# Performance work log

Measured on AMD Instinct MI355X. Metric: run time of the kernel, lower is better.

The kernel has to match this reference:

```python
import jax, jax.numpy as jnp
import numpy as np


def setup_inputs() -> dict:
    key = jax.random.key(0)
    ks = jax.random.split(key, 8)
    B, S, Nc, C, Cseed = 4, 4096, 8192, 512, 256
    return {
        "query_xyz": jax.random.normal(ks[0], (B, S, 3), dtype=jnp.float32),
        "ref_xyz": jax.random.normal(ks[1], (B, Nc, 3), dtype=jnp.float32),
        "ref_feat": jax.random.normal(ks[2], (B, C, Nc), dtype=jnp.float32),
        "seed_features": jax.random.normal(ks[3], (B, Cseed, S), dtype=jnp.float32),
        "W_seed_proj": jax.random.normal(ks[4], (Cseed, C), dtype=jnp.float32) * 0.02,
        "b_seed_proj": jax.random.normal(ks[5], (Cseed,), dtype=jnp.float32) * 0.02,
        "W_concat_proj": jax.random.normal(ks[6], (Cseed, 2 * Cseed), dtype=jnp.float32) * 0.02,
        "b_concat_proj": jax.random.normal(ks[7], (Cseed,), dtype=jnp.float32) * 0.02,
    }


def _nn_gather(query_xyz, ref_xyz, ref_feat):
    # torch.cdist(p=2) + argmin: argmin over squared distance is identical
    # (sqrt is monotonic), so we skip the sqrt.
    q2 = jnp.sum(query_xyz * query_xyz, axis=-1, keepdims=True)      # (B,S,1)
    r2 = jnp.sum(ref_xyz * ref_xyz, axis=-1)[:, None, :]             # (B,1,Nc)
    qr = jnp.einsum("bsd,bnd->bsn", query_xyz, ref_xyz)              # (B,S,Nc)
    d2 = q2 + r2 - 2.0 * qr                                          # (B,S,Nc)
    idx = jnp.argmin(d2, axis=-1)                                    # (B,S) int
    # gather nearest-neighbor features: (B,C,Nc) -> (B,C,S)
    return jnp.take_along_axis(ref_feat, idx[:, None, :], axis=2)


def reference(query_xyz, ref_xyz, ref_feat, seed_features,
              W_seed_proj, b_seed_proj, W_concat_proj, b_concat_proj):
    lift3d_raw = _nn_gather(query_xyz, ref_xyz, ref_feat)            # (B,C,S)
    # 1x1 Conv1d == channel matmul
    lift3d_seed = jnp.einsum("oc,bcs->bos", W_seed_proj, lift3d_raw) \
                  + b_seed_proj[None, :, None]                       # (B,256,S)
    fused = jnp.concatenate([seed_features, lift3d_seed], axis=1)    # (B,512,S)
    out = jnp.einsum("oc,bcs->bos", W_concat_proj, fused) \
          + b_concat_proj[None, :, None]                             # (B,256,S)
    return out
```

## Files before the change

### kernel.cpp

```cpp
#include <hip/hip_runtime.h>

#define B_   4
#define S_   4096
#define NC   8192
#define C_   512
#define CS   256
#define KTOT 768

typedef __attribute__((ext_vector_type(8))) short short8;
typedef __attribute__((ext_vector_type(4))) float f32x4;

static __device__ __forceinline__ unsigned short f2bf(float x) {
    unsigned u = __builtin_bit_cast(unsigned, x);
    unsigned r = u + 0x7FFFu + ((u >> 16) & 1u);
    return (unsigned short)(r >> 16);
}

__global__ __launch_bounds__(256) void pad_ref_kernel(const float* __restrict__ rxyz,
                                                      float4* __restrict__ refpk) {
    int gid = blockIdx.x * 256 + threadIdx.x;
    float x = rxyz[gid * 3 + 0];
    float y = rxyz[gid * 3 + 1];
    float z = rxyz[gid * 3 + 2];
    float r2 = __fadd_rn(__fadd_rn(__fmul_rn(x, x), __fmul_rn(y, y)), __fmul_rn(z, z));
    refpk[gid] = make_float4(x, y, z, r2);
}

__global__ __launch_bounds__(256) void argmin_partial_kernel(
        const float* __restrict__ qxyz, const float4* __restrict__ refpk,
        float* __restrict__ pval, int* __restrict__ pidx) {
    int tid = threadIdx.x;
    int lane = tid & 63;
    int qg = tid >> 6;
    int sblk = blockIdx.x;
    int c = blockIdx.y;
    int b = blockIdx.z;
    int sbase = sblk * 32 + qg * 8;

    float qx[8], qy[8], qz[8], q2[8];
    #pragma unroll
    for (int q = 0; q < 8; ++q) {
        const float* qp = qxyz + ((size_t)(b * S_ + sbase + q)) * 3;
        qx[q] = qp[0]; qy[q] = qp[1]; qz[q] = qp[2];
        q2[q] = __fadd_rn(__fadd_rn(__fmul_rn(qx[q], qx[q]), __fmul_rn(qy[q], qy[q])),
                          __fmul_rn(qz[q], qz[q]));
    }

    const float4* ep = refpk + (size_t)b * NC + c * 2048 + lane;
    float best[8];
    int bj[8];
    #pragma unroll
    for (int q = 0; q < 8; ++q) { best[q] = 3.4028235e38f; bj[q] = 0; }

    #pragma unroll 4
    for (int j = 0; j < 32; ++j) {
        float4 r = ep[j * 64];
        #pragma unroll
        for (int q = 0; q < 8; ++q) {
            float qr = __fadd_rn(__fadd_rn(__fmul_rn(qx[q], r.x), __fmul_rn(qy[q], r.y)),
                                 __fmul_rn(qz[q], r.z));
            float d2 = __fsub_rn(__fadd_rn(q2[q], r.w), __fadd_rn(qr, qr));
            if (d2 < best[q]) { best[q] = d2; bj[q] = j; }
        }
    }

    __shared__ float sv[64][33];
    __shared__ int   sx[64][33];
    #pragma unroll
    for (int q = 0; q < 8; ++q) {
        sv[lane][qg * 8 + q] = best[q];
        sx[lane][qg * 8 + q] = c * 2048 + bj[q] * 64 + lane;
    }
    __syncthreads();
    if (tid < 32) {
        float v = sv[0][tid];
        int x = sx[0][tid];
        #pragma unroll 8
        for (int l = 1; l < 64; ++l) {
            float vv = sv[l][tid];
            int xx = sx[l][tid];
            if (vv < v || (vv == v && xx < x)) { v = vv; x = xx; }
        }
        int qs = b * S_ + sblk * 32 + tid;
        pval[qs * 4 + c] = v;
        pidx[qs * 4 + c] = x;
    }
}

__global__ __launch_bounds__(256) void transpose_kernel(const float* __restrict__ rf,
                                                        unsigned short* __restrict__ refT) {
    __shared__ float t[64][65];
    int tid = threadIdx.x;
    int b = blockIdx.z;
    int c0 = blockIdx.y * 64;
    int n0 = blockIdx.x * 64;
    int tx = tid & 15, ty = tid >> 4;
    #pragma unroll
    for (int r = 0; r < 4; ++r) {
        int c = r * 16 + ty;
        float4 v = *(const float4*)(rf + ((size_t)b * C_ + c0 + c) * NC + n0 + tx * 4);
        t[tx * 4 + 0][c] = v.x;
        t[tx * 4 + 1][c] = v.y;
        t[tx * 4 + 2][c] = v.z;
        t[tx * 4 + 3][c] = v.w;
    }
    __syncthreads();
    #pragma unroll
    for (int r = 0; r < 4; ++r) {
        int n = r * 16 + ty;
        ushort4 o;
        o.x = f2bf(t[n][tx * 4 + 0]);
        o.y = f2bf(t[n][tx * 4 + 1]);
        o.z = f2bf(t[n][tx * 4 + 2]);
        o.w = f2bf(t[n][tx * 4 + 3]);
        *(ushort4*)(refT + ((size_t)b * NC + n0 + n) * C_ + c0 + tx * 4) = o;
    }
}

__global__ __launch_bounds__(256) void wc_kernel(const float* __restrict__ Wcat,
                                                 const float* __restrict__ Wseed,
                                                 unsigned short* __restrict__ Wcomb) {
    __shared__ float sa[64][68];
    __shared__ float sbt[64][68];
    int tid = threadIdx.x;
    int to = blockIdx.y * 64;
    int tc = blockIdx.x * 64;
    int tx = tid & 15, ty = tid >> 4;
    float acc[4][4] = {};
    for (int kt = 0; kt < 256; kt += 64) {
        __syncthreads();
        #pragma unroll
        for (int r = 0; r < 4; ++r) {
            int oo = r * 16 + ty;
            float4 v = *(const float4*)(Wcat + (size_t)(to + oo) * 512 + 256 + kt + tx * 4);
            sa[oo][tx * 4 + 0] = v.x;
            sa[oo][tx * 4 + 1] = v.y;
            sa[oo][tx * 4 + 2] = v.z;
            sa[oo][tx * 4 + 3] = v.w;
            float4 u = *(const float4*)(Wseed + (size_t)(kt + oo) * 512 + tc + tx * 4);
            sbt[oo][tx * 4 + 0] = u.x;
            sbt[oo][tx * 4 + 1] = u.y;
            sbt[oo][tx * 4 + 2] = u.z;
            sbt[oo][tx * 4 + 3] = u.w;
        }
        __syncthreads();
        for (int k = 0; k < 64; ++k) {
            float a[4], bb[4];
            #pragma unroll
            for (int i = 0; i < 4; ++i) a[i] = sa[ty * 4 + i][k];
            #pragma unroll
            for (int j = 0; j < 4; ++j) bb[j] = sbt[k][tx * 4 + j];
            #pragma unroll
            for (int i = 0; i < 4; ++i)
                #pragma unroll
                for (int j = 0; j < 4; ++j)
                    acc[i][j] = fmaf(a[i], bb[j], acc[i][j]);
        }
    }
    #pragma unroll
    for (int i = 0; i < 4; ++i)
        #pragma unroll
        for (int j = 0; j < 4; ++j)
            Wcomb[(size_t)(to + ty * 4 + i) * KTOT + 256 + tc + tx * 4 + j] = f2bf(acc[i][j]);
}

__global__ __launch_bounds__(256) void w1_kernel(const float* __restrict__ Wcat,
                                                 unsigned short* __restrict__ Wcomb) {
    int gid = blockIdx.x * 256 + threadIdx.x;
    int o = gid >> 8, c = gid & 255;
    Wcomb[(size_t)o * KTOT + c] = f2bf(Wcat[(size_t)o * 512 + c]);
}

__global__ __launch_bounds__(64) void beff_kernel(const float* __restrict__ Wcat,
                                                  const float* __restrict__ bseed,
                                                  const float* __restrict__ bcat,
                                                  float* __restrict__ beff) {
    int o = blockIdx.x;
    int l = threadIdx.x;
    float4 w = *(const float4*)(Wcat + (size_t)o * 512 + 256 + l * 4);
    float4 bb = *(const float4*)(bseed + l * 4);
    float acc = __fmul_rn(w.x, bb.x);
    acc = fmaf(w.y, bb.y, acc);
    acc = fmaf(w.z, bb.z, acc);
    acc = fmaf(w.w, bb.w, acc);
    #pragma unroll
    for (int off = 32; off > 0; off >>= 1)
        acc += __shfl_down(acc, off);
    if (l == 0) beff[o] = acc + bcat[o];
}

__global__ __launch_bounds__(256) void fused_gemm_kernel(
        const unsigned short* __restrict__ Wcomb,
        const float* __restrict__ seed,
        const unsigned short* __restrict__ refT,
        const float* __restrict__ pval,
        const int* __restrict__ pidx,
        const float* __restrict__ beff,
        float* __restrict__ out) {
    __shared__ __align__(16) unsigned short sA[128][72];
    __shared__ __align__(16) unsigned short sB[32][72];
    __shared__ int sIdx[32];
    __shared__ float sBias[128];

    int tid = threadIdx.x;
    int b = blockIdx.z;
    int m0 = blockIdx.y * 128;
    int s0 = blockIdx.x * 32;
    if (tid < 32) {
        int qs = b * S_ + s0 + tid;
        float v = pval[qs * 4 + 0];
        int x = pidx[qs * 4 + 0];
        #pragma unroll
        for (int c = 1; c < 4; ++c) {
            float vv = pval[qs * 4 + c];
            int xx = pidx[qs * 4 + c];
            if (vv < v || (vv == v && xx < x)) { v = vv; x = xx; }
        }
        sIdx[tid] = x & (NC - 1);
    }
    if (tid < 128) sBias[tid] = beff[m0 + tid];

    int lane = tid & 63;
    int w = tid >> 6;
    int ln = lane & 15;
    int quad = lane >> 4;
    int q8 = quad * 8;

    f32x4 acc[2][2];
    #pragma unroll
    for (int i = 0; i < 2; ++i)
        #pragma unroll
        for (int j = 0; j < 2; ++j)
            acc[i][j] = (f32x4){0.f, 0.f, 0.f, 0.f};

    for (int ks = 0; ks < 12; ++ks) {
        int k0 = ks * 64;
        __syncthreads();
        #pragma unroll
        for (int i = 0; i < 4; ++i) {
            int ch = tid + 256 * i;
            int mm = ch >> 3;
            int kk8 = (ch & 7) << 3;
            *(short8*)&sA[mm][kk8] =
                *(const short8*)(Wcomb + (size_t)(m0 + mm) * KTOT + k0 + kk8);
        }
        if (k0 < 256) {
            int n = tid & 31;
            int kk8 = (tid >> 5) << 3;
            const float* sp = seed + ((size_t)b * CS + k0 + kk8) * S_ + s0 + n;
            unsigned short tmp[8];
            #pragma unroll
            for (int r = 0; r < 8; ++r)
                tmp[r] = f2bf(sp[(size_t)r * S_]);
            *(short8*)&sB[n][kk8] = *(const short8*)tmp;
        } else {
            int n = tid >> 3;
            int kk8 = (tid & 7) << 3;
            const unsigned short* gp =
                refT + ((size_t)b * NC + sIdx[n]) * C_ + (k0 - 256) + kk8;
            *(short8*)&sB[n][kk8] = *(const short8*)gp;
        }
        __syncthreads();
        #pragma unroll
        for (int kf = 0; kf < 2; ++kf) {
            short8 af[2], bfr[2];
            #pragma unroll
            for (int i = 0; i < 2; ++i)
                af[i] = *(const short8*)&sA[w * 32 + i * 16 + ln][kf * 32 + q8];
            #pragma unroll
            for (int j = 0; j < 2; ++j)
                bfr[j] = *(const short8*)&sB[j * 16 + ln][kf * 32 + q8];
            #pragma unroll
            for (int i = 0; i < 2; ++i)
                #pragma unroll
                for (int j = 0; j < 2; ++j)
                    acc[i][j] = __builtin_amdgcn_mfma_f32_16x16x32_bf16(af[i], bfr[j], acc[i][j], 0, 0, 0);
        }
    }

    #pragma unroll
    for (int i = 0; i < 2; ++i) {
        int mb = w * 32 + i * 16 + quad * 4;
        #pragma unroll
        for (int j = 0; j < 2; ++j) {
            int col = s0 + j * 16 + ln;
            #pragma unroll
            for (int r = 0; r < 4; ++r) {
                int m = mb + r;
                out[((size_t)b * CS + m0 + m) * S_ + col] = acc[i][j][r] + sBias[m];
            }
        }
    }
}

extern "C" void kernel_launch(void* const* d_in, const int* in_sizes, int n_in,
                              void* d_out, int out_size, void* d_ws, size_t ws_size,
                              hipStream_t stream) {
    const float* qxyz  = (const float*)d_in[0];
    const float* rxyz  = (const float*)d_in[1];
    const float* rfeat = (const float*)d_in[2];
    const float* seed  = (const float*)d_in[3];
    const float* Wseed = (const float*)d_in[4];
    const float* bseed = (const float*)d_in[5];
    const float* Wcat  = (const float*)d_in[6];
    const float* bcat  = (const float*)d_in[7];
    float* out = (float*)d_out;

    char* ws = (char*)d_ws;
    float* pval           = (float*)(ws);
    int* pidx             = (int*)(ws + 262144);
    float* beff           = (float*)(ws + 524288);
    float4* refpk         = (float4*)(ws + 528384);
    unsigned short* Wcomb = (unsigned short*)(ws + 1052672);
    unsigned short* refT  = (unsigned short*)(ws + 1445888);

    hipLaunchKernelGGL(pad_ref_kernel,        dim3(128),       dim3(256), 0, stream, rxyz, refpk);
    hipLaunchKernelGGL(argmin_partial_kernel, dim3(128, 4, 4), dim3(256), 0, stream,
                       qxyz, refpk, pval, pidx);
    hipLaunchKernelGGL(transpose_kernel,      dim3(128, 8, 4), dim3(256), 0, stream, rfeat, refT);
    hipLaunchKernelGGL(wc_kernel,             dim3(8, 4),      dim3(256), 0, stream, Wcat, Wseed, Wcomb);
    hipLaunchKernelGGL(w1_kernel,             dim3(256),       dim3(256), 0, stream, Wcat, Wcomb);
    hipLaunchKernelGGL(beff_kernel,           dim3(256),       dim3(64),  0, stream, Wcat, bseed, bcat, beff);
    hipLaunchKernelGGL(fused_gemm_kernel,     dim3(128, 2, 4), dim3(256), 0, stream,
                       Wcomb, seed, refT, pval, pidx, beff, out);
}
```

Baseline: 214.4 us.

## Merge prep and mid-stage kernels into two launches with interleaved work

Combines the four small preparation kernels (bias fold, weight product, weight cast, ref padding) into one launch split by block index. The argmin and the feature transpose/bf16 cast are merged into one kernel whose blocks interleave 1:2, so compute-bound argmin overlaps with memory-bound transpose. The argmin's cross-lane reduction now uses wave shuffles instead of shared memory, and the distance uses an fma. The aim is to cut launch overhead and idle tails between stages; the fma can change rounding and so possibly which neighbor wins a tie.

```diff
diff --git a/kernel.cpp b/kernel.cpp
--- a/kernel.cpp
+++ b/kernel.cpp
@@ -16,177 +16,182 @@
     return (unsigned short)(r >> 16);
 }
 
-__global__ __launch_bounds__(256) void pad_ref_kernel(const float* __restrict__ rxyz,
-                                                      float4* __restrict__ refpk) {
-    int gid = blockIdx.x * 256 + threadIdx.x;
-    float x = rxyz[gid * 3 + 0];
-    float y = rxyz[gid * 3 + 1];
-    float z = rxyz[gid * 3 + 2];
-    float r2 = __fadd_rn(__fadd_rn(__fmul_rn(x, x), __fmul_rn(y, y)), __fmul_rn(z, z));
-    refpk[gid] = make_float4(x, y, z, r2);
-}
-
-__global__ __launch_bounds__(256) void argmin_partial_kernel(
-        const float* __restrict__ qxyz, const float4* __restrict__ refpk,
-        float* __restrict__ pval, int* __restrict__ pidx) {
-    int tid = threadIdx.x;
-    int lane = tid & 63;
-    int qg = tid >> 6;
-    int sblk = blockIdx.x;
-    int c = blockIdx.y;
-    int b = blockIdx.z;
-    int sbase = sblk * 32 + qg * 8;
-
-    float qx[8], qy[8], qz[8], q2[8];
-    #pragma unroll
-    for (int q = 0; q < 8; ++q) {
-        const float* qp = qxyz + ((size_t)(b * S_ + sbase + q)) * 3;
-        qx[q] = qp[0]; qy[q] = qp[1]; qz[q] = qp[2];
-        q2[q] = __fadd_rn(__fadd_rn(__fmul_rn(qx[q], qx[q]), __fmul_rn(qy[q], qy[q])),
-                          __fmul_rn(qz[q], qz[q]));
-    }
-
-    const float4* ep = refpk + (size_t)b * NC + c * 2048 + lane;
-    float best[8];
-    int bj[8];
-    #pragma unroll
-    for (int q = 0; q < 8; ++q) { best[q] = 3.4028235e38f; bj[q] = 0; }
-
-    #pragma unroll 4
-    for (int j = 0; j < 32; ++j) {
-        float4 r = ep[j * 64];
-        #pragma unroll
-        for (int q = 0; q < 8; ++q) {
-            float qr = __fadd_rn(__fadd_rn(__fmul_rn(qx[q], r.x), __fmul_rn(qy[q], r.y)),
-                                 __fmul_rn(qz[q], r.z));
-            float d2 = __fsub_rn(__fadd_rn(q2[q], r.w), __fadd_rn(qr, qr));
-            if (d2 < best[q]) { best[q] = d2; bj[q] = j; }
-        }
-    }
-
-    __shared__ float sv[64][33];
-    __shared__ int   sx[64][33];
-    #pragma unroll
-    for (int q = 0; q < 8; ++q) {
-        sv[lane][qg * 8 + q] = best[q];
-        sx[lane][qg * 8 + q] = c * 2048 + bj[q] * 64 + lane;
-    }
-    __syncthreads();
-    if (tid < 32) {
-        float v = sv[0][tid];
-        int x = sx[0][tid];
-        #pragma unroll 8
-        for (int l = 1; l < 64; ++l) {
-            float vv = sv[l][tid];
-            int xx = sx[l][tid];
-            if (vv < v || (vv == v && xx < x)) { v = vv; x = xx; }
-        }
-        int qs = b * S_ + sblk * 32 + tid;
-        pval[qs * 4 + c] = v;
-        pidx[qs * 4 + c] = x;
-    }
-}
-
-__global__ __launch_bounds__(256) void transpose_kernel(const float* __restrict__ rf,
-                                                        unsigned short* __restrict__ refT) {
-    __shared__ float t[64][65];
-    int tid = threadIdx.x;
-    int b = blockIdx.z;
-    int c0 = blockIdx.y * 64;
-    int n0 = blockIdx.x * 64;
-    int tx = tid & 15, ty = tid >> 4;
-    #pragma unroll
-    for (int r = 0; r < 4; ++r) {
-        int c = r * 16 + ty;
-        float4 v = *(const float4*)(rf + ((size_t)b * C_ + c0 + c) * NC + n0 + tx * 4);
-        t[tx * 4 + 0][c] = v.x;
-        t[tx * 4 + 1][c] = v.y;
-        t[tx * 4 + 2][c] = v.z;
-        t[tx * 4 + 3][c] = v.w;
-    }
-    __syncthreads();
-    #pragma unroll
-    for (int r = 0; r < 4; ++r) {
-        int n = r * 16 + ty;
-        ushort4 o;
-        o.x = f2bf(t[n][tx * 4 + 0]);
-        o.y = f2bf(t[n][tx * 4 + 1]);
-        o.z = f2bf(t[n][tx * 4 + 2]);
-        o.w = f2bf(t[n][tx * 4 + 3]);
-        *(ushort4*)(refT + ((size_t)b * NC + n0 + n) * C_ + c0 + tx * 4) = o;
-    }
-}
-
-__global__ __launch_bounds__(256) void wc_kernel(const float* __restrict__ Wcat,
-                                                 const float* __restrict__ Wseed,
-                                                 unsigned short* __restrict__ Wcomb) {
+__global__ __launch_bounds__(256) void prep_kernel(
+        const float* __restrict__ rxyz, float4* __restrict__ refpk,
+        const float* __restrict__ Wcat, const float* __restrict__ Wseed,
+        unsigned short* __restrict__ Wcomb,
+        const float* __restrict__ bseed, const float* __restrict__ bcat,
+        float* __restrict__ beff) {
     __shared__ float sa[64][68];
     __shared__ float sbt[64][68];
+    int bid = blockIdx.x;
     int tid = threadIdx.x;
-    int to = blockIdx.y * 64;
-    int tc = blockIdx.x * 64;
-    int tx = tid & 15, ty = tid >> 4;
-    float acc[4][4] = {};
-    for (int kt = 0; kt < 256; kt += 64) {
+
+    if (bid < 64) {
+        int w = tid >> 6, l = tid & 63;
+        int o = bid * 4 + w;
+        float4 wv = *(const float4*)(Wcat + (size_t)o * 512 + 256 + l * 4);
+        float4 bb = *(const float4*)(bseed + l * 4);
+        float acc = __fmul_rn(wv.x, bb.x);
+        acc = fmaf(wv.y, bb.y, acc);
+        acc = fmaf(wv.z, bb.z, acc);
+        acc = fmaf(wv.w, bb.w, acc);
+        #pragma unroll
+        for (int off = 32; off > 0; off >>= 1) acc += __shfl_down(acc, off);
+        if (l == 0) beff[o] = acc + bcat[o];
+    } else if (bid < 96) {
+        int xb = bid - 64;
+        int tc = (xb & 7) * 64;
+        int to = (xb >> 3) * 64;
+        int tx = tid & 15, ty = tid >> 4;
+        float acc[4][4] = {};
+        for (int kt = 0; kt < 256; kt += 64) {
+            __syncthreads();
+            #pragma unroll
+            for (int r = 0; r < 4; ++r) {
+                int oo = r * 16 + ty;
+                float4 v = *(const float4*)(Wcat + (size_t)(to + oo) * 512 + 256 + kt + tx * 4);
+                sa[oo][tx * 4 + 0] = v.x;
+                sa[oo][tx * 4 + 1] = v.y;
+                sa[oo][tx * 4 + 2] = v.z;
+                sa[oo][tx * 4 + 3] = v.w;
+                float4 u = *(const float4*)(Wseed + (size_t)(kt + oo) * 512 + tc + tx * 4);
+                sbt[oo][tx * 4 + 0] = u.x;
+                sbt[oo][tx * 4 + 1] = u.y;
+                sbt[oo][tx * 4 + 2] = u.z;
+                sbt[oo][tx * 4 + 3] = u.w;
+            }
+            __syncthreads();
+            for (int k = 0; k < 64; ++k) {
+                float a[4], bb2[4];
+                #pragma unroll
+                for (int i = 0; i < 4; ++i) a[i] = sa[ty * 4 + i][k];
+                #pragma unroll
+                for (int j = 0; j < 4; ++j) bb2[j] = sbt[k][tx * 4 + j];
+                #pragma unroll
+                for (int i = 0; i < 4; ++i)
+                    #pragma unroll
+                    for (int j = 0; j < 4; ++j)
+                        acc[i][j] = fmaf(a[i], bb2[j], acc[i][j]);
+            }
+        }
+        #pragma unroll
+        for (int i = 0; i < 4; ++i)
+            #pragma unroll
+            for (int j = 0; j < 4; ++j)
+                Wcomb[(size_t)(to + ty * 4 + i) * KTOT + 256 + tc + tx * 4 + j] = f2bf(acc[i][j]);
+    } else if (bid < 160) {
+        int g = ((bid - 96) * 256 + tid) * 4;
+        int o = g >> 8, cc = g & 255;
+        float4 v = *(const float4*)(Wcat + (size_t)o * 512 + cc);
+        ushort4 ov;
+        ov.x = f2bf(v.x); ov.y = f2bf(v.y); ov.z = f2bf(v.z); ov.w = f2bf(v.w);
+        *(ushort4*)(Wcomb + (size_t)o * KTOT + cc) = ov;
+    } else {
+        int gid = (bid - 160) * 256 + tid;
+        float x = rxyz[gid * 3 + 0];
+        float y = rxyz[gid * 3 + 1];
+        float z = rxyz[gid * 3 + 2];
+        float r2 = __fadd_rn(__fadd_rn(__fmul_rn(x, x), __fmul_rn(y, y)), __fmul_rn(z, z));
+        refpk[gid] = make_float4(x, y, z, r2);
+    }
+}
+
+__global__ __launch_bounds__(256) void mid_kernel(
+        const float* __restrict__ qxyz, const float4* __restrict__ refpk,
+        float* __restrict__ pval, int* __restrict__ pidx,
+        const float* __restrict__ rf, unsigned short* __restrict__ refT) {
+    __shared__ float t[64][65];
+    int bid = blockIdx.x;
+    int tid = threadIdx.x;
+
+    if (bid % 3 != 0) {
+        int id = bid - bid / 3 - 1;
+        int b = id >> 10;
+        int c0 = ((id >> 7) & 7) * 64;
+        int n0 = (id & 127) * 64;
+        int tx = tid & 15, ty = tid >> 4;
+        #pragma unroll
+        for (int r = 0; r < 4; ++r) {
+            int cc = r * 16 + ty;
+            float4 v = *(const float4*)(rf + ((size_t)b * C_ + c0 + cc) * NC + n0 + tx * 4);
+            t[tx * 4 + 0][cc] = v.x;
+            t[tx * 4 + 1][cc] = v.y;
+            t[tx * 4 + 2][cc] = v.z;
+            t[tx * 4 + 3][cc] = v.w;
+        }
         __syncthreads();
         #pragma unroll
         for (int r = 0; r < 4; ++r) {
-            int oo = r * 16 + ty;
-            float4 v = *(const float4*)(Wcat + (size_t)(to + oo) * 512 + 256 + kt + tx * 4);
-            sa[oo][tx * 4 + 0] = v.x;
-            sa[oo][tx * 4 + 1] = v.y;
-            sa[oo][tx * 4 + 2] = v.z;
-            sa[oo][tx * 4 + 3] = v.w;
-            float4 u = *(const float4*)(Wseed + (size_t)(kt + oo) * 512 + tc + tx * 4);
-            sbt[oo][tx * 4 + 0] = u.x;
-            sbt[oo][tx * 4 + 1] = u.y;
-            sbt[oo][tx * 4 + 2] = u.z;
-            sbt[oo][tx * 4 + 3] = u.w;
-        }
-        __syncthreads();
-        for (int k = 0; k < 64; ++k) {
-            float a[4], bb[4];
-            #pragma unroll
-            for (int i = 0; i < 4; ++i) a[i] = sa[ty * 4 + i][k];
-            #pragma unroll
-            for (int j = 0; j < 4; ++j) bb[j] = sbt[k][tx * 4 + j];
-            #pragma unroll
-            for (int i = 0; i < 4; ++i)
-                #pragma unroll
-                for (int j = 0; j < 4; ++j)
-                    acc[i][j] = fmaf(a[i], bb[j], acc[i][j]);
-        }
-    }
-    #pragma unroll
-    for (int i = 0; i < 4; ++i)
-        #pragma unroll
-        for (int j = 0; j < 4; ++j)
-            Wcomb[(size_t)(to + ty * 4 + i) * KTOT + 256 + tc + tx * 4 + j] = f2bf(acc[i][j]);
-}
-
-__global__ __launch_bounds__(256) void w1_kernel(const float* __restrict__ Wcat,
-                                                 unsigned short* __restrict__ Wcomb) {
-    int gid = blockIdx.x * 256 + threadIdx.x;
-    int o = gid >> 8, c = gid & 255;
-    Wcomb[(size_t)o * KTOT + c] = f2bf(Wcat[(size_t)o * 512 + c]);
-}
-
-__global__ __launch_bounds__(64) void beff_kernel(const float* __restrict__ Wcat,
-                                                  const float* __restrict__ bseed,
-                                                  const float* __restrict__ bcat,
-                                                  float* __restrict__ beff) {
-    int o = blockIdx.x;
-    int l = threadIdx.x;
-    float4 w = *(const float4*)(Wcat + (size_t)o * 512 + 256 + l * 4);
-    float4 bb = *(const float4*)(bseed + l * 4);
-    float acc = __fmul_rn(w.x, bb.x);
-    acc = fmaf(w.y, bb.y, acc);
-    acc = fmaf(w.z, bb.z, acc);
-    acc = fmaf(w.w, bb.w, acc);
-    #pragma unroll
-    for (int off = 32; off > 0; off >>= 1)
-        acc += __shfl_down(acc, off);
-    if (l == 0) beff[o] = acc + bcat[o];
+            int n = r * 16 + ty;
+            ushort4 o;
+            o.x = f2bf(t[n][tx * 4 + 0]);
+            o.y = f2bf(t[n][tx * 4 + 1]);
+            o.z = f2bf(t[n][tx * 4 + 2]);
+            o.w = f2bf(t[n][tx * 4 + 3]);
+            *(ushort4*)(refT + ((size_t)b * NC + n0 + n) * C_ + c0 + tx * 4) = o;
+        }
+    } else {
+        int aid = bid / 3;
+        int sblk = aid & 127;
+        int c = (aid >> 7) & 3;
+        int b = aid >> 9;
+        int lane = tid & 63;
+        int qg = tid >> 6;
+        int sbase = sblk * 32 + qg * 8;
+
+        float qx[8], qy[8], qz[8], q2[8];
+        #pragma unroll
+        for (int q = 0; q < 8; ++q) {
+            const float* qp = qxyz + ((size_t)(b * S_ + sbase + q)) * 3;
+            qx[q] = qp[0]; qy[q] = qp[1]; qz[q] = qp[2];
+            q2[q] = __fadd_rn(__fadd_rn(__fmul_rn(qx[q], qx[q]), __fmul_rn(qy[q], qy[q])),
+                              __fmul_rn(qz[q], qz[q]));
+        }
+
+        const float4* ep = refpk + (size_t)b * NC + c * 2048 + lane;
+        float best[8];
+        int bj[8];
+        #pragma unroll
+        for (int q = 0; q < 8; ++q) { best[q] = 3.4028235e38f; bj[q] = 0; }
+
+        #pragma unroll 4
+        for (int j = 0; j < 32; ++j) {
+            float4 r = ep[j * 64];
+            #pragma unroll
+            for (int q = 0; q < 8; ++q) {
+                float qr = __fadd_rn(__fadd_rn(__fmul_rn(qx[q], r.x), __fmul_rn(qy[q], r.y)),
+                                     __fmul_rn(qz[q], r.z));
+                float s = __fadd_rn(q2[q], r.w);
+                float d2 = fmaf(qr, -2.0f, s);
+                if (d2 < best[q]) { best[q] = d2; bj[q] = j; }
+            }
+        }
+
+        int bx[8];
+        #pragma unroll
+        for (int q = 0; q < 8; ++q) bx[q] = c * 2048 + bj[q] * 64 + lane;
+
+        #pragma unroll
+        for (int m = 1; m < 64; m <<= 1) {
+            #pragma unroll
+            for (int q = 0; q < 8; ++q) {
+                float vv = __shfl_xor(best[q], m, 64);
+                int xx = __shfl_xor(bx[q], m, 64);
+                if (vv < best[q] || (vv == best[q] && xx < bx[q])) {
+                    best[q] = vv; bx[q] = xx;
+                }
+            }
+        }
+        if (lane == 0) {
+            #pragma unroll
+            for (int q = 0; q < 8; ++q) {
+                int qs = b * S_ + sbase + q;
+                pval[qs * 4 + c] = best[q];
+                pidx[qs * 4 + c] = bx[q];
+            }
+        }
+    }
 }
 
 __global__ __launch_bounds__(256) void fused_gemm_kernel(
@@ -314,13 +319,10 @@
     unsigned short* Wcomb = (unsigned short*)(ws + 1052672);
     unsigned short* refT  = (unsigned short*)(ws + 1445888);
 
-    hipLaunchKernelGGL(pad_ref_kernel,        dim3(128),       dim3(256), 0, stream, rxyz, refpk);
-    hipLaunchKernelGGL(argmin_partial_kernel, dim3(128, 4, 4), dim3(256), 0, stream,
-                       qxyz, refpk, pval, pidx);
-    hipLaunchKernelGGL(transpose_kernel,      dim3(128, 8, 4), dim3(256), 0, stream, rfeat, refT);
-    hipLaunchKernelGGL(wc_kernel,             dim3(8, 4),      dim3(256), 0, stream, Wcat, Wseed, Wcomb);
-    hipLaunchKernelGGL(w1_kernel,             dim3(256),       dim3(256), 0, stream, Wcat, Wcomb);
-    hipLaunchKernelGGL(beff_kernel,           dim3(256),       dim3(64),  0, stream, Wcat, bseed, bcat, beff);
-    hipLaunchKernelGGL(fused_gemm_kernel,     dim3(128, 2, 4), dim3(256), 0, stream,
+    hipLaunchKernelGGL(prep_kernel, dim3(288), dim3(256), 0, stream,
+                       rxyz, refpk, Wcat, Wseed, Wcomb, bseed, bcat, beff);
+    hipLaunchKernelGGL(mid_kernel, dim3(6144), dim3(256), 0, stream,
+                       qxyz, refpk, pval, pidx, rfeat, refT);
+    hipLaunchKernelGGL(fused_gemm_kernel, dim3(128, 2, 4), dim3(256), 0, stream,
                        Wcomb, seed, refT, pval, pidx, beff, out);
 }
```

After: 188.4 us. 1.14x faster.
